# Kernel optimization log

Hardware: AMD Instinct MI355X
Metric: run time of the kernel (lower is better)

Reference implementation:

```python
import jax, jax.numpy as jnp
import numpy as np

N = 50000      # nodes
E = 800000     # edges (avg degree 16)
DIM = 64       # embedding_dim == out_dim
H = 2          # num_heads
HID = 128      # hidden_dim of filter network
NG = 64        # n_gaussians
RC = 5.0       # cosine cutoff radius (cutoffFunc)
LOG2 = float(np.log(2.0))


def ssp(v):
    # shifted softplus: softplus(x) - ln(2)
    return jax.nn.softplus(v) - LOG2


def cosine_cutoff(r):
    return 0.5 * (jnp.cos(jnp.pi * r / RC) + 1.0) * (r < RC)


def setup_inputs() -> dict:
    key = jax.random.key(0)
    ks = jax.random.split(key, 16)
    x = jax.random.normal(ks[0], (N, DIM), jnp.float32)
    gs = jax.random.uniform(ks[1], (E, NG), jnp.float32)
    rij = jax.random.uniform(ks[2], (E,), jnp.float32) * RC
    src = jax.random.randint(ks[3], (E,), 0, N)
    dst = jax.random.randint(ks[4], (E,), 0, N)
    def w(k, shape, fan_in):
        return jax.random.normal(k, shape, jnp.float32) * (1.0 / np.sqrt(fan_in))
    return {
        "x": x, "gs": gs, "rij": rij, "src": src, "dst": dst,
        "fc_w": w(ks[5], (DIM, H * DIM), DIM),          # node projection (no bias, GAT style)
        "attn_l": w(ks[6], (H, DIM), DIM),
        "attn_r": w(ks[7], (H, DIM), DIM),
        "filt_w1": w(ks[8], (NG, HID), NG),             # filter net on gaussian-expanded dists
        "filt_b1": jnp.zeros((HID,), jnp.float32),
        "filt_w2": w(ks[9], (HID, H * DIM), HID),
        "filt_b2": jnp.zeros((H * DIM,), jnp.float32),
        "mlp_w1": w(ks[10], (H * DIM, DIM), H * DIM),   # Dense(embedding_dim*num_heads, embedding_dim)
        "mlp_b1": jnp.zeros((DIM,), jnp.float32),
        "mlp_w2": w(ks[11], (DIM, DIM), DIM),           # Dense(embedding_dim, embedding_dim)
        "mlp_b2": jnp.zeros((DIM,), jnp.float32),
    }


def reference(x, gs, rij, src, dst, fc_w, attn_l, attn_r,
              filt_w1, filt_b1, filt_w2, filt_b2,
              mlp_w1, mlp_b1, mlp_w2, mlp_b2):
    n = x.shape[0]
    # --- MPGATConv ---
    feat = (x @ fc_w).reshape(n, H, DIM)                     # [N,H,D]
    el = jnp.sum(feat * attn_l, axis=-1)                     # [N,H]
    er = jnp.sum(feat * attn_r, axis=-1)                     # [N,H]
    e = jax.nn.leaky_relu(el[src] + er[dst], 0.2)            # [E,H] edge scores
    # neighbor-wise (per destination node) softmax, numerically stable
    m = jax.ops.segment_max(e, dst, num_segments=n)          # [N,H]
    m = jnp.where(jnp.isfinite(m), m, 0.0)
    ex = jnp.exp(e - m[dst])                                 # [E,H]
    den = jax.ops.segment_sum(ex, dst, num_segments=n)       # [N,H]
    alpha = ex / jnp.maximum(den[dst], 1e-16)                # [E,H]
    # continuous-filter from gaussian-expanded distances + cosine cutoff
    filt = (ssp(gs @ filt_w1 + filt_b1) @ filt_w2 + filt_b2).reshape(-1, H, DIM)  # [E,H,D]
    coef = alpha * cosine_cutoff(rij)[:, None]               # [E,H]
    msg = feat[src] * filt * coef[:, :, None]                # [E,H,D]
    agg = jax.ops.segment_sum(msg, dst, num_segments=n)      # [N,H,D]
    res = ssp(agg).reshape(n, H * DIM)                       # activation + head concat
    # --- MLP head: Dense+ssp, Dense ---
    res = ssp(res @ mlp_w1 + mlp_b1) @ mlp_w2 + mlp_b2       # [N,DIM]
    return res
```

## Files before the change

kernel.cpp:

```cpp
#include <hip/hip_runtime.h>
#include <hip/hip_fp16.h>
#include <math.h>

typedef _Float16 half8 __attribute__((ext_vector_type(8)));
typedef float f32x4 __attribute__((ext_vector_type(4)));

__device__ __forceinline__ float sspf(float v) {
    float t = __expf(-fabsf(v));
    return fmaxf(v, 0.0f) + __logf(1.0f + t) - 0.693147180559945f;
}

__global__ __launch_bounds__(256) void prep_weights(const float* __restrict__ w1,
    const float* __restrict__ w2, _Float16* __restrict__ w1t, _Float16* __restrict__ w2t) {
    int i = blockIdx.x * 256 + threadIdx.x;
    if (i < 64 * 128) {
        int n = i >> 6, k = i & 63;
        w1t[i] = (_Float16)w1[k * 128 + n];
    }
    int j = i - 64 * 128;
    if (j >= 0 && j < 128 * 128) {
        int n = j >> 7, k = j & 127;
        w2t[j] = (_Float16)w2[k * 128 + n];
    }
}

__global__ __launch_bounds__(256) void node_proj(const float* __restrict__ x,
    const float* __restrict__ fcw, const float* __restrict__ al, const float* __restrict__ ar,
    _Float16* __restrict__ featH, float* __restrict__ el, float* __restrict__ er, int N) {
    __shared__ float xs[64][65];
    __shared__ float pl[4][64], pr[4][64];
    const int tid = threadIdx.x, lane = tid & 63, w = tid >> 6;
    const int n0 = blockIdx.x * 64;
    const int nrows = min(64, N - n0);
    {
        int r = tid >> 2, c0 = (tid & 3) * 16;
        if (r < nrows) {
            const float4* p = (const float4*)(x + (size_t)(n0 + r) * 64 + c0);
            #pragma unroll
            for (int q = 0; q < 4; ++q) {
                float4 v = p[q];
                xs[r][c0 + q * 4 + 0] = v.x; xs[r][c0 + q * 4 + 1] = v.y;
                xs[r][c0 + q * 4 + 2] = v.z; xs[r][c0 + q * 4 + 3] = v.w;
            }
        }
    }
    __syncthreads();
    const int c0w = w * 32;
    float acc[32];
    #pragma unroll
    for (int c = 0; c < 32; ++c) acc[c] = 0.f;
    #pragma unroll 4
    for (int k = 0; k < 64; ++k) {
        float xv = xs[lane][k];
        const float* wr = &fcw[k * 128 + c0w];
        #pragma unroll
        for (int c = 0; c < 32; ++c) acc[c] = fmaf(xv, wr[c], acc[c]);
    }
    if (lane < nrows) {
        _Float16* fp = featH + (size_t)(n0 + lane) * 128 + c0w;
        #pragma unroll
        for (int c = 0; c < 32; ++c) fp[c] = (_Float16)acc[c];
    }
    float vl = 0.f, vr = 0.f;
    #pragma unroll
    for (int c = 0; c < 32; ++c) {
        vl = fmaf(acc[c], al[c0w + c], vl);
        vr = fmaf(acc[c], ar[c0w + c], vr);
    }
    pl[w][lane] = vl; pr[w][lane] = vr;
    __syncthreads();
    if (w == 0 && lane < nrows)
        ((float2*)el)[n0 + lane] = make_float2(pl[0][lane] + pl[1][lane],
                                               pl[2][lane] + pl[3][lane]);
    if (w == 1 && lane < nrows)
        ((float2*)er)[n0 + lane] = make_float2(pr[0][lane] + pr[1][lane],
                                               pr[2][lane] + pr[3][lane]);
}

__global__ void edge_sm(const int* __restrict__ src, const int* __restrict__ dst,
    const float* __restrict__ el, const float* __restrict__ er,
    float* __restrict__ exb, float* __restrict__ den, int E) {
    int e = blockIdx.x * 256 + threadIdx.x;
    if (e >= E) return;
    int s = src[e], d = dst[e];
    float2 a = ((const float2*)el)[s];
    float2 b = ((const float2*)er)[d];
    float e0 = a.x + b.x; e0 = (e0 > 0.f) ? e0 : 0.2f * e0;
    float e1 = a.y + b.y; e1 = (e1 > 0.f) ? e1 : 0.2f * e1;
    float x0 = __expf(e0), x1 = __expf(e1);
    ((float2*)exb)[e] = make_float2(x0, x1);
    unsafeAtomicAdd(&den[2 * d],     x0);
    unsafeAtomicAdd(&den[2 * d + 1], x1);
}

__global__ __launch_bounds__(256) void edge_filter_mfma(
    const float* __restrict__ gs, const float* __restrict__ rij,
    const int* __restrict__ src, const int* __restrict__ dst,
    const _Float16* __restrict__ w1t, const float* __restrict__ b1,
    const _Float16* __restrict__ w2t, const float* __restrict__ b2,
    const _Float16* __restrict__ featH, const float* __restrict__ exs,
    const float* __restrict__ den, float* __restrict__ agg) {
    __shared__ _Float16 sGS[64][72];
    __shared__ _Float16 sH[64][136];
    __shared__ float coefs[2][64];
    __shared__ int ssrc[64], sdst[64];
    const int tid  = threadIdx.x;
    const int lane = tid & 63;
    const int w    = tid >> 6;
    const int e0   = blockIdx.x * 64;
    const int ln   = lane & 15;
    const int kq   = (lane >> 4) * 8;

    if (w == 0) {
        int e = e0 + lane;
        int sv = src[e], dv = dst[e];
        ssrc[lane] = sv; sdst[lane] = dv;
        float rv = rij[e];
        float cut = (rv < 5.0f) ? 0.5f * (cosf(0.6283185307179586f * rv) + 1.0f) : 0.0f;
        float2 exv = ((const float2*)exs)[e];
        float2 dnv = ((const float2*)den)[dv];
        coefs[0][lane] = exv.x / fmaxf(dnv.x, 1e-16f) * cut;
        coefs[1][lane] = exv.y / fmaxf(dnv.y, 1e-16f) * cut;
    }
    {
        int r = tid >> 2, c0 = (tid & 3) * 16;
        const float4* g4 = (const float4*)(gs + (size_t)(e0 + r) * 64 + c0);
        #pragma unroll
        for (int q = 0; q < 4; ++q) {
            float4 v = g4[q];
            sGS[r][c0 + q * 4 + 0] = (_Float16)v.x;
            sGS[r][c0 + q * 4 + 1] = (_Float16)v.y;
            sGS[r][c0 + q * 4 + 2] = (_Float16)v.z;
            sGS[r][c0 + q * 4 + 3] = (_Float16)v.w;
        }
    }
    __syncthreads();

    const int mrow = (w << 4) + ln;

    f32x4 acc[8];
    #pragma unroll
    for (int nt = 0; nt < 8; ++nt) acc[nt] = (f32x4){0.f, 0.f, 0.f, 0.f};
    #pragma unroll
    for (int kk = 0; kk < 2; ++kk) {
        half8 a = *(const half8*)&sGS[mrow][kk * 32 + kq];
        #pragma unroll
        for (int nt = 0; nt < 8; ++nt) {
            half8 b = *(const half8*)&w1t[(nt * 16 + ln) * 64 + kk * 32 + kq];
            acc[nt] = __builtin_amdgcn_mfma_f32_16x16x32_f16(a, b, acc[nt], 0, 0, 0);
        }
    }
    #pragma unroll
    for (int nt = 0; nt < 8; ++nt) {
        int col = nt * 16 + ln;
        float bias = b1[col];
        #pragma unroll
        for (int r = 0; r < 4; ++r) {
            int erow = (w << 4) + ((lane >> 4) << 2) + r;
            sH[erow][col] = (_Float16)sspf(acc[nt][r] + bias);
        }
    }

    f32x4 facc[8];
    #pragma unroll
    for (int nt = 0; nt < 8; ++nt) facc[nt] = (f32x4){0.f, 0.f, 0.f, 0.f};
    #pragma unroll
    for (int kk = 0; kk < 4; ++kk) {
        half8 a = *(const half8*)&sH[mrow][kk * 32 + kq];
        #pragma unroll
        for (int nt = 0; nt < 8; ++nt) {
            half8 b = *(const half8*)&w2t[(nt * 16 + ln) * 128 + kk * 32 + kq];
            facc[nt] = __builtin_amdgcn_mfma_f32_16x16x32_f16(a, b, facc[nt], 0, 0, 0);
        }
    }

    #pragma unroll
    for (int nt = 0; nt < 8; ++nt) {
        int col = nt * 16 + ln;
        float bias = b2[col];
        int h = col >> 6;
        #pragma unroll
        for (int r = 0; r < 4; ++r) {
            int erow = (w << 4) + ((lane >> 4) << 2) + r;
            float F = facc[nt][r] + bias;
            float cf = coefs[h][erow];
            int s = ssrc[erow], d = sdst[erow];
            float msg = (float)featH[(size_t)s * 128 + col] * F * cf;
            unsafeAtomicAdd(&agg[(size_t)d * 128 + col], msg);
        }
    }
}

__global__ __launch_bounds__(256) void out_head(const float* __restrict__ agg,
    const float* __restrict__ w1, const float* __restrict__ b1,
    const float* __restrict__ w2, const float* __restrict__ b2,
    float* __restrict__ out, int N) {
    __shared__ float a2[64][129];
    __shared__ float ts[64][65];
    const int tid = threadIdx.x, lane = tid & 63, w = tid >> 6;
    const int n0 = blockIdx.x * 64;
    const int nrows = min(64, N - n0);
    {
        int r = tid >> 2, c0 = (tid & 3) * 32;
        if (r < nrows) {
            const float4* p = (const float4*)(agg + (size_t)(n0 + r) * 128 + c0);
            #pragma unroll
            for (int q = 0; q < 8; ++q) {
                float4 v = p[q];
                a2[r][c0 + q * 4 + 0] = sspf(v.x); a2[r][c0 + q * 4 + 1] = sspf(v.y);
                a2[r][c0 + q * 4 + 2] = sspf(v.z); a2[r][c0 + q * 4 + 3] = sspf(v.w);
            }
        }
    }
    __syncthreads();
    const int c0w = w * 16;
    float acc[16];
    #pragma unroll
    for (int c = 0; c < 16; ++c) acc[c] = b1[c0w + c];
    #pragma unroll 4
    for (int k = 0; k < 128; ++k) {
        float av = a2[lane][k];
        const float* wr = &w1[k * 64 + c0w];
        #pragma unroll
        for (int c = 0; c < 16; ++c) acc[c] = fmaf(av, wr[c], acc[c]);
    }
    #pragma unroll
    for (int c = 0; c < 16; ++c) ts[lane][c0w + c] = sspf(acc[c]);
    __syncthreads();
    float o[16];
    #pragma unroll
    for (int c = 0; c < 16; ++c) o[c] = b2[c0w + c];
    #pragma unroll 4
    for (int k = 0; k < 64; ++k) {
        float av = ts[lane][k];
        const float* wr = &w2[k * 64 + c0w];
        #pragma unroll
        for (int c = 0; c < 16; ++c) o[c] = fmaf(av, wr[c], o[c]);
    }
    if (lane < nrows) {
        float* op = out + (size_t)(n0 + lane) * 64 + c0w;
        #pragma unroll
        for (int q = 0; q < 4; ++q)
            ((float4*)op)[q] = make_float4(o[q*4], o[q*4+1], o[q*4+2], o[q*4+3]);
    }
}

extern "C" void kernel_launch(void* const* d_in, const int* in_sizes, int n_in,
                              void* d_out, int out_size, void* d_ws, size_t ws_size,
                              hipStream_t stream) {
    const float* x   = (const float*)d_in[0];
    const float* gs  = (const float*)d_in[1];
    const float* rij = (const float*)d_in[2];
    const int*   src = (const int*)d_in[3];
    const int*   dst = (const int*)d_in[4];
    const float* fcw = (const float*)d_in[5];
    const float* al  = (const float*)d_in[6];
    const float* ar  = (const float*)d_in[7];
    const float* fw1 = (const float*)d_in[8];
    const float* fb1 = (const float*)d_in[9];
    const float* fw2 = (const float*)d_in[10];
    const float* fb2 = (const float*)d_in[11];
    const float* mw1 = (const float*)d_in[12];
    const float* mb1 = (const float*)d_in[13];
    const float* mw2 = (const float*)d_in[14];
    const float* mb2 = (const float*)d_in[15];
    float* outp = (float*)d_out;

    const int N = in_sizes[0] / 64;
    const int E = in_sizes[2];

    _Float16* featH = (_Float16*)d_ws;
    float*    el  = (float*)(featH + (size_t)N * 128);
    float*    er  = el  + (size_t)N * 2;
    float*    exb = er  + (size_t)N * 2;
    float*    den = exb + (size_t)E * 2;
    float*    agg = den + (size_t)N * 2;
    _Float16* w1t = (_Float16*)(agg + (size_t)N * 128);
    _Float16* w2t = w1t + 64 * 128;

    hipMemsetAsync(den, 0, (size_t)N * 130 * sizeof(float), stream);

    prep_weights    <<<96, 256, 0, stream>>>(fw1, fw2, w1t, w2t);
    node_proj       <<<(N + 63) / 64, 256, 0, stream>>>(x, fcw, al, ar, featH, el, er, N);
    edge_sm         <<<(E + 255) / 256, 256, 0, stream>>>(src, dst, el, er, exb, den, E);
    edge_filter_mfma<<<E / 64, 256, 0, stream>>>(gs, rij, src, dst, w1t, fb1, w2t, fb2,
                                                 featH, exb, den, agg);
    out_head        <<<(N + 63) / 64, 256, 0, stream>>>(agg, mw1, mb1, mw2, mb2, outp, N);
}
```

Baseline: 1.053 ms.

## Sort edges by destination and fuse softmax into filter kernel with segmented atomics

```diff
diff --git a/kernel.cpp b/kernel.cpp
--- a/kernel.cpp
+++ b/kernel.cpp
@@ -22,6 +22,59 @@
         int n = j >> 7, k = j & 127;
         w2t[j] = (_Float16)w2[k * 128 + n];
     }
+}
+
+__global__ void hist_dst(const int* __restrict__ dst, int* __restrict__ deg, int E) {
+    int e = blockIdx.x * 256 + threadIdx.x;
+    if (e < E) atomicAdd(&deg[dst[e]], 1);
+}
+
+__global__ __launch_bounds__(1024) void scan_exclusive(const int* __restrict__ deg,
+    int* __restrict__ base, int n) {
+    __shared__ int wsum[16];
+    __shared__ int carry_s;
+    const int t = threadIdx.x, lane = t & 63, wv = t >> 6;
+    if (t == 0) carry_s = 0;
+    __syncthreads();
+    const int nch = (n + 1023) >> 10;
+    for (int ch = 0; ch < nch; ++ch) {
+        int i = (ch << 10) + t;
+        int v = (i < n) ? deg[i] : 0;
+        int inc = v;
+        #pragma unroll
+        for (int off = 1; off < 64; off <<= 1) {
+            int u = __shfl_up(inc, off);
+            if (lane >= off) inc += u;
+        }
+        if (lane == 63) wsum[wv] = inc;
+        __syncthreads();
+        if (wv == 0) {
+            int s = (lane < 16) ? wsum[lane] : 0;
+            #pragma unroll
+            for (int off = 1; off < 16; off <<= 1) {
+                int u = __shfl_up(s, off);
+                if (lane >= off) s += u;
+            }
+            if (lane < 16) wsum[lane] = s;
+        }
+        __syncthreads();
+        int carry = carry_s;
+        int excl = carry + inc - v + (wv ? wsum[wv - 1] : 0);
+        if (i < n) base[i] = excl;
+        int total = wsum[15];
+        __syncthreads();
+        if (t == 0) carry_s = carry + total;
+        __syncthreads();
+    }
+}
+
+__global__ void scatter_perm(const int* __restrict__ dst, const int* __restrict__ base,
+    int* __restrict__ cnt, int* __restrict__ perm, int E) {
+    int e = blockIdx.x * 256 + threadIdx.x;
+    if (e >= E) return;
+    int d = dst[e];
+    int p = base[d] + atomicAdd(&cnt[d], 1);
+    perm[p] = e;
 }
 
 __global__ __launch_bounds__(256) void node_proj(const float* __restrict__ x,
@@ -77,32 +130,18 @@
                                                pr[2][lane] + pr[3][lane]);
 }
 
-__global__ void edge_sm(const int* __restrict__ src, const int* __restrict__ dst,
-    const float* __restrict__ el, const float* __restrict__ er,
-    float* __restrict__ exb, float* __restrict__ den, int E) {
-    int e = blockIdx.x * 256 + threadIdx.x;
-    if (e >= E) return;
-    int s = src[e], d = dst[e];
-    float2 a = ((const float2*)el)[s];
-    float2 b = ((const float2*)er)[d];
-    float e0 = a.x + b.x; e0 = (e0 > 0.f) ? e0 : 0.2f * e0;
-    float e1 = a.y + b.y; e1 = (e1 > 0.f) ? e1 : 0.2f * e1;
-    float x0 = __expf(e0), x1 = __expf(e1);
-    ((float2*)exb)[e] = make_float2(x0, x1);
-    unsafeAtomicAdd(&den[2 * d],     x0);
-    unsafeAtomicAdd(&den[2 * d + 1], x1);
-}
-
 __global__ __launch_bounds__(256) void edge_filter_mfma(
     const float* __restrict__ gs, const float* __restrict__ rij,
     const int* __restrict__ src, const int* __restrict__ dst,
+    const int* __restrict__ perm,
     const _Float16* __restrict__ w1t, const float* __restrict__ b1,
     const _Float16* __restrict__ w2t, const float* __restrict__ b2,
-    const _Float16* __restrict__ featH, const float* __restrict__ exs,
-    const float* __restrict__ den, float* __restrict__ agg) {
+    const _Float16* __restrict__ featH, const float* __restrict__ el,
+    const float* __restrict__ er, float* __restrict__ den, float* __restrict__ agg) {
     __shared__ _Float16 sGS[64][72];
     __shared__ _Float16 sH[64][136];
     __shared__ float coefs[2][64];
+    __shared__ int seid[64];
     __shared__ int ssrc[64], sdst[64];
     const int tid  = threadIdx.x;
     const int lane = tid & 63;
@@ -111,20 +150,28 @@
     const int ln   = lane & 15;
     const int kq   = (lane >> 4) * 8;
 
+    if (tid < 64) seid[tid] = perm[e0 + tid];
+    __syncthreads();
+
     if (w == 0) {
-        int e = e0 + lane;
-        int sv = src[e], dv = dst[e];
+        int eid = seid[lane];
+        int sv = src[eid], dv = dst[eid];
         ssrc[lane] = sv; sdst[lane] = dv;
-        float rv = rij[e];
+        float rv = rij[eid];
         float cut = (rv < 5.0f) ? 0.5f * (cosf(0.6283185307179586f * rv) + 1.0f) : 0.0f;
-        float2 exv = ((const float2*)exs)[e];
-        float2 dnv = ((const float2*)den)[dv];
-        coefs[0][lane] = exv.x / fmaxf(dnv.x, 1e-16f) * cut;
-        coefs[1][lane] = exv.y / fmaxf(dnv.y, 1e-16f) * cut;
+        float2 a = ((const float2*)el)[sv];
+        float2 b = ((const float2*)er)[dv];
+        float s0 = a.x + b.x; s0 = (s0 > 0.f) ? s0 : 0.2f * s0;
+        float s1 = a.y + b.y; s1 = (s1 > 0.f) ? s1 : 0.2f * s1;
+        float x0 = __expf(s0), x1 = __expf(s1);
+        unsafeAtomicAdd(&den[2 * dv],     x0);
+        unsafeAtomicAdd(&den[2 * dv + 1], x1);
+        coefs[0][lane] = x0 * cut;
+        coefs[1][lane] = x1 * cut;
     }
     {
         int r = tid >> 2, c0 = (tid & 3) * 16;
-        const float4* g4 = (const float4*)(gs + (size_t)(e0 + r) * 64 + c0);
+        const float4* g4 = (const float4*)(gs + (size_t)seid[r] * 64 + c0);
         #pragma unroll
         for (int q = 0; q < 4; ++q) {
             float4 v = g4[q];
@@ -173,25 +220,41 @@
             facc[nt] = __builtin_amdgcn_mfma_f32_16x16x32_f16(a, b, facc[nt], 0, 0, 0);
         }
     }
-
     #pragma unroll
     for (int nt = 0; nt < 8; ++nt) {
         int col = nt * 16 + ln;
         float bias = b2[col];
-        int h = col >> 6;
         #pragma unroll
         for (int r = 0; r < 4; ++r) {
             int erow = (w << 4) + ((lane >> 4) << 2) + r;
-            float F = facc[nt][r] + bias;
-            float cf = coefs[h][erow];
-            int s = ssrc[erow], d = sdst[erow];
-            float msg = (float)featH[(size_t)s * 128 + col] * F * cf;
-            unsafeAtomicAdd(&agg[(size_t)d * 128 + col], msg);
-        }
+            sH[erow][col] = (_Float16)(facc[nt][r] + bias);
+        }
+    }
+    __syncthreads();
+
+    {
+        const int col  = tid & 127;
+        const int r0   = (tid >> 7) * 32;
+        const int hsel = col >> 6;
+        float acc2 = 0.f;
+        int dprev = sdst[r0];
+        #pragma unroll 8
+        for (int r = r0; r < r0 + 32; ++r) {
+            int dcur = sdst[r];
+            if (dcur != dprev) {
+                unsafeAtomicAdd(&agg[(size_t)dprev * 128 + col], acc2);
+                acc2 = 0.f; dprev = dcur;
+            }
+            float fv = (float)sH[r][col];
+            float m  = fv * coefs[hsel][r] * (float)featH[(size_t)ssrc[r] * 128 + col];
+            acc2 += m;
+        }
+        unsafeAtomicAdd(&agg[(size_t)dprev * 128 + col], acc2);
     }
 }
 
 __global__ __launch_bounds__(256) void out_head(const float* __restrict__ agg,
+    const float* __restrict__ den,
     const float* __restrict__ w1, const float* __restrict__ b1,
     const float* __restrict__ w2, const float* __restrict__ b2,
     float* __restrict__ out, int N) {
@@ -203,12 +266,16 @@
     {
         int r = tid >> 2, c0 = (tid & 3) * 32;
         if (r < nrows) {
+            int h = c0 >> 6;
+            float inv = 1.0f / fmaxf(den[(size_t)(n0 + r) * 2 + h], 1e-16f);
             const float4* p = (const float4*)(agg + (size_t)(n0 + r) * 128 + c0);
             #pragma unroll
             for (int q = 0; q < 8; ++q) {
                 float4 v = p[q];
-                a2[r][c0 + q * 4 + 0] = sspf(v.x); a2[r][c0 + q * 4 + 1] = sspf(v.y);
-                a2[r][c0 + q * 4 + 2] = sspf(v.z); a2[r][c0 + q * 4 + 3] = sspf(v.w);
+                a2[r][c0 + q * 4 + 0] = sspf(v.x * inv);
+                a2[r][c0 + q * 4 + 1] = sspf(v.y * inv);
+                a2[r][c0 + q * 4 + 2] = sspf(v.z * inv);
+                a2[r][c0 + q * 4 + 3] = sspf(v.w * inv);
             }
         }
     }
@@ -270,20 +337,25 @@
     const int E = in_sizes[2];
 
     _Float16* featH = (_Float16*)d_ws;
-    float*    el  = (float*)(featH + (size_t)N * 128);
-    float*    er  = el  + (size_t)N * 2;
-    float*    exb = er  + (size_t)N * 2;
-    float*    den = exb + (size_t)E * 2;
-    float*    agg = den + (size_t)N * 2;
-    _Float16* w1t = (_Float16*)(agg + (size_t)N * 128);
-    _Float16* w2t = w1t + 64 * 128;
-
-    hipMemsetAsync(den, 0, (size_t)N * 130 * sizeof(float), stream);
+    float*    el   = (float*)(featH + (size_t)N * 128);
+    float*    er   = el   + (size_t)N * 2;
+    float*    den  = er   + (size_t)N * 2;
+    float*    agg  = den  + (size_t)N * 2;
+    int*      deg  = (int*)(agg + (size_t)N * 128);
+    int*      cnt  = deg  + N;
+    int*      base = cnt  + N;
+    int*      perm = base + N;
+    _Float16* w1t  = (_Float16*)(perm + E);
+    _Float16* w2t  = w1t + 64 * 128;
+
+    hipMemsetAsync(den, 0, (size_t)N * 132 * sizeof(float), stream);
 
     prep_weights    <<<96, 256, 0, stream>>>(fw1, fw2, w1t, w2t);
+    hist_dst        <<<(E + 255) / 256, 256, 0, stream>>>(dst, deg, E);
+    scan_exclusive  <<<1, 1024, 0, stream>>>(deg, base, N);
+    scatter_perm    <<<(E + 255) / 256, 256, 0, stream>>>(dst, base, cnt, perm, E);
     node_proj       <<<(N + 63) / 64, 256, 0, stream>>>(x, fcw, al, ar, featH, el, er, N);
-    edge_sm         <<<(E + 255) / 256, 256, 0, stream>>>(src, dst, el, er, exb, den, E);
-    edge_filter_mfma<<<E / 64, 256, 0, stream>>>(gs, rij, src, dst, w1t, fb1, w2t, fb2,
-                                                 featH, exb, den, agg);
-    out_head        <<<(N + 63) / 64, 256, 0, stream>>>(agg, mw1, mb1, mw2, mb2, outp, N);
-}
+    edge_filter_mfma<<<E / 64, 256, 0, stream>>>(gs, rij, src, dst, perm, w1t, fb1,
+                                                 w2t, fb2, featH, el, er, den, agg);
+    out_head        <<<(N + 63) / 64, 256, 0, stream>>>(agg, den, mw1, mb1, mw2, mb2, outp, N);
+}
```

Result: no change. 1.059 ms (+0.6%).
